# Kernel tuning notes

Hardware: AMD Instinct MI355X
Metric: run time of the kernel (lower is better)

The kernel has to match this reference:

```python
import jax, jax.numpy as jnp
import numpy as np

N = 50000   # nodes
E = 600000  # edges (avg degree 12)
F = 16      # raw node features
P = 32      # n_channels_preproc
C = 128     # n_channels
L = 6       # n_gnn_layers
LBL = 2     # n_labels


def _dense_init(k, fan_in, shape):
    return (jax.random.normal(k, shape, jnp.float32) / np.float32(np.sqrt(fan_in)))


def setup_inputs() -> dict:
    key = jax.random.key(0)
    ks = jax.random.split(key, 12)
    return {
        "x": jax.random.normal(ks[0], (N, F), jnp.float32),
        "edge_src": jax.random.randint(ks[1], (E,), 0, N, dtype=jnp.int32),
        "edge_dst": jax.random.randint(ks[2], (E,), 0, N, dtype=jnp.int32),
        "edge_weight": jax.random.uniform(ks[3], (E,), jnp.float32),  # normalized-adjacency values
        "preproc_W": _dense_init(ks[4], F, (F, P)), "preproc_b": jnp.zeros((P,), jnp.float32),
        "fc_in1_W": _dense_init(ks[5], P, (P, C)), "fc_in1_b": jnp.zeros((C,), jnp.float32),
        "fc_in2_W": _dense_init(ks[6], P, (P, C)), "fc_in2_b": jnp.zeros((C,), jnp.float32),
        "gcn_W": _dense_init(ks[7], C, (L, C, C)), "gcn_b": jnp.zeros((L, C), jnp.float32),
        "fcg_W": _dense_init(ks[8], 2 * C, (L, 2 * C, C)), "fcg_b": jnp.zeros((L, C), jnp.float32),
        "last1_W": _dense_init(ks[9], 2 * C, (2 * C, C)), "last1_b": jnp.zeros((C,), jnp.float32),
        "last2_W": _dense_init(ks[10], C, (C, LBL)), "last2_b": jnp.zeros((LBL,), jnp.float32),
    }


def reference(x, edge_src, edge_dst, edge_weight,
              preproc_W, preproc_b, fc_in1_W, fc_in1_b, fc_in2_W, fc_in2_b,
              gcn_W, gcn_b, fcg_W, fcg_b, last1_W, last1_b, last2_W, last2_b):
    relu = jax.nn.relu
    h = relu(x @ preproc_W + preproc_b)                      # preproc Dense
    node_id = relu(h @ fc_in1_W + fc_in1_b)                  # node identity branch
    h = relu(h @ fc_in2_W + fc_in2_b)

    def layer(h, params):
        W, b, Wf, bf = params
        # GCNConv: act(A_hat @ (h @ W) + b), A_hat as COO edge list
        hw = h @ W                                           # [N, C]
        msg = hw[edge_src] * edge_weight[:, None]            # [E, C]
        agg = jax.ops.segment_sum(msg, edge_dst, num_segments=N)
        g = relu(agg + b)
        merged = jnp.concatenate([node_id, g], axis=-1)      # [N, 2C]
        return relu(merged @ Wf + bf), None                  # dropout = identity (eval)

    h, _ = jax.lax.scan(layer, h, (gcn_W, gcn_b, fcg_W, fcg_b))

    merged = jnp.concatenate([node_id, h], axis=-1)
    h = relu(merged @ last1_W + last1_b)
    return jax.nn.sigmoid(h @ last2_W + last2_b)             # [N, n_labels]
```

## Files before the change

### kernel.cpp

```cpp
#include <hip/hip_runtime.h>
#include <cstddef>
#include <cstdint>

#define NN 50000
#define NE 600000
#define NB 391

typedef __attribute__((ext_vector_type(8))) short bf16x8;
typedef __attribute__((ext_vector_type(4))) float f32x4;

#define SWZ(x) (((x) ^ ((x) >> 2)) & 3)

#define GLDS16(src, dst)                                                     \
    __builtin_amdgcn_global_load_lds(                                        \
        (const __attribute__((address_space(1))) void*)(src),                \
        (__attribute__((address_space(3))) void*)(dst), 16, 0, 0)

__device__ __forceinline__ float bf2f(ushort u) {
    return __uint_as_float(((uint32_t)u) << 16);
}
__device__ __forceinline__ ushort f2bf(float f) {
    uint32_t b = __float_as_uint(f);
    return (ushort)((b + 0x7FFF + ((b >> 16) & 1)) >> 16);
}

__global__ __launch_bounds__(256)
void convbh_kernel(const float* __restrict__ f1W, const float* __restrict__ f2W,
                   const float* __restrict__ gW, const float* __restrict__ fgW,
                   const float* __restrict__ l1W, ushort* __restrict__ wt,
                   const int* __restrict__ dst, int* __restrict__ bcnt)
{
    if (blockIdx.x < 1312) {
        int i = blockIdx.x * 256 + threadIdx.x;
        if (i >= 335872) return;
        float v;
        if (i < 4096) {
            int c = i >> 5, k = i & 31;
            v = f1W[k * 128 + c];
        } else if (i < 8192) {
            int j = i - 4096; int c = j >> 5, k = j & 31;
            v = f2W[k * 128 + c];
        } else if (i < 8192 + 98304) {
            int j = i - 8192; int l = j >> 14, r = j & 16383;
            int c = r >> 7, k = r & 127;
            v = gW[l * 16384 + k * 128 + c];
        } else if (i < 8192 + 98304 + 196608) {
            int j = i - (8192 + 98304); int l = j >> 15, r = j & 32767;
            int c = r >> 8, k = r & 255;
            v = fgW[l * 32768 + k * 128 + c];
        } else {
            int j = i - (8192 + 98304 + 196608);
            int c = j >> 8, k = j & 255;
            v = l1W[k * 128 + c];
        }
        wt[i] = f2bf(v);
    } else {
        __shared__ int h[NB];
        int tx = threadIdx.x;
        for (int i = tx; i < NB; i += 256) h[i] = 0;
        __syncthreads();
        int e0 = (blockIdx.x - 1312) * 1024;
#pragma unroll
        for (int k = 0; k < 4; ++k) {
            int e = e0 + k * 256 + tx;
            if (e < NE) atomicAdd(&h[dst[e] >> 7], 1);
        }
        __syncthreads();
        for (int i = tx; i < NB; i += 256)
            if (h[i]) atomicAdd(&bcnt[i], h[i]);
    }
}

__global__ __launch_bounds__(512)
void bscan_kernel(const int* __restrict__ bcnt, int* __restrict__ bbase,
                  int* __restrict__ bcur)
{
    __shared__ int buf[512];
    int t = threadIdx.x;
    int v = (t < NB) ? bcnt[t] : 0;
    buf[t] = v;
    __syncthreads();
    for (int s = 1; s < 512; s <<= 1) {
        int u = (t >= s) ? buf[t - s] : 0;
        __syncthreads();
        buf[t] += u;
        __syncthreads();
    }
    if (t < NB) {
        int ex = buf[t] - v;
        bbase[t] = ex;
        bcur[t]  = ex;
    }
    if (t == 0) bbase[NB] = NE;
}

__global__ __launch_bounds__(256)
void pass1_kernel(const int* __restrict__ src, const int* __restrict__ dst,
                  const float* __restrict__ w, int* __restrict__ bcur,
                  unsigned int* __restrict__ stage_pk,
                  unsigned char* __restrict__ stage_dl)
{
    __shared__ int cnt[NB];
    __shared__ int gbase[NB];
    int tx = threadIdx.x;
    for (int i = tx; i < NB; i += 256) cnt[i] = 0;
    __syncthreads();
    int e0 = blockIdx.x * 1024;
    int myd[4], myrank[4];
    unsigned int mypk[4];
#pragma unroll
    for (int k = 0; k < 4; ++k) {
        int e = e0 + k * 256 + tx;
        if (e < NE) {
            int d = dst[e];
            myd[k]    = d;
            mypk[k]   = (unsigned int)src[e] | ((unsigned int)f2bf(w[e]) << 17);
            myrank[k] = atomicAdd(&cnt[d >> 7], 1);
        } else {
            myd[k] = -1;
        }
    }
    __syncthreads();
    for (int i = tx; i < NB; i += 256)
        gbase[i] = cnt[i] ? atomicAdd(&bcur[i], cnt[i]) : 0;
    __syncthreads();
#pragma unroll
    for (int k = 0; k < 4; ++k) {
        if (myd[k] >= 0) {
            int p = gbase[myd[k] >> 7] + myrank[k];
            stage_pk[p] = mypk[k];
            stage_dl[p] = (unsigned char)(myd[k] & 127);
        }
    }
}

__global__ __launch_bounds__(256)
void p2pre_kernel(const unsigned int* __restrict__ stage_pk,
                  const unsigned char* __restrict__ stage_dl,
                  const int* __restrict__ bbase,
                  unsigned int* __restrict__ esw, int* __restrict__ off,
                  const float* __restrict__ x, const float* __restrict__ preW,
                  const float* __restrict__ preb, ushort* __restrict__ h0b)
{
    if (blockIdx.x < NB) {
        __shared__ int h[128];
        __shared__ int lofs[128];
        int b    = blockIdx.x;
        int tx   = threadIdx.x;
        int base = bbase[b];
        int cnt  = bbase[b + 1] - base;
        if (tx < 128) h[tx] = 0;
        __syncthreads();
        for (int i = tx; i < cnt; i += 256)
            atomicAdd(&h[stage_dl[base + i]], 1);
        __syncthreads();
        if (tx == 0) {
            int run = 0;
            for (int i = 0; i < 128; ++i) { lofs[i] = run; run += h[i]; }
        }
        __syncthreads();
        int node0 = b * 128;
        if (tx < 128) {
            int n = node0 + tx;
            if (n < NN) off[n] = base + lofs[tx];
            h[tx] = 0;
        }
        if (b == NB - 1 && tx == 0) off[NN] = NE;
        __syncthreads();
        for (int i = tx; i < cnt; i += 256) {
            int d = stage_dl[base + i];
            int r = atomicAdd(&h[d], 1);
            esw[base + lofs[d] + r] = stage_pk[base + i];
        }
    } else {
        __shared__ float Wl[512];
        __shared__ float bl[32];
        int tx = threadIdx.x;
        Wl[tx]       = preW[tx];
        Wl[tx + 256] = preW[tx + 256];
        if (tx < 32) bl[tx] = preb[tx];
        __syncthreads();
        int n = (blockIdx.x - NB) * 256 + tx;
        if (n >= NN) return;
        float xr[16];
        const float4* xp = (const float4*)(x + (size_t)n * 16);
#pragma unroll
        for (int q = 0; q < 4; ++q) {
            float4 v = xp[q];
            xr[q*4+0]=v.x; xr[q*4+1]=v.y; xr[q*4+2]=v.z; xr[q*4+3]=v.w;
        }
        float acc[32];
#pragma unroll
        for (int c = 0; c < 32; ++c) acc[c] = bl[c];
#pragma unroll
        for (int k = 0; k < 16; ++k)
#pragma unroll
            for (int c = 0; c < 32; ++c)
                acc[c] = fmaf(xr[k], Wl[k*32+c], acc[c]);
        ushort4* op = (ushort4*)(h0b + (size_t)n * 32);
#pragma unroll
        for (int q = 0; q < 8; ++q) {
            ushort4 v;
            v.x = f2bf(fmaxf(acc[q*4+0], 0.f));
            v.y = f2bf(fmaxf(acc[q*4+1], 0.f));
            v.z = f2bf(fmaxf(acc[q*4+2], 0.f));
            v.w = f2bf(fmaxf(acc[q*4+3], 0.f));
            op[q] = v;
        }
    }
}

__global__ __launch_bounds__(128)
void fc1f0_kernel(const ushort* __restrict__ h0b,
                  const ushort* __restrict__ wf1, const float* __restrict__ f1b,
                  ushort* __restrict__ nidb,
                  const ushort* __restrict__ wf2, const float* __restrict__ f2b,
                  const ushort* __restrict__ wg, ushort* __restrict__ hwb)
{
    __shared__ ushort Atile[64 * 32];
    __shared__ ushort Btile[128 * 32];
    __shared__ ushort Xt[64 * 128];
    const int tx   = threadIdx.x;
    const int wave = tx >> 6;
    const int lane = tx & 63;
    const int rs  = lane >> 2;
    const int chn = (lane & 3) ^ SWZ(rs);
    const int m    = lane & 15;
    const int quad = lane >> 4;
    const int slot = quad ^ SWZ(m);

    if (blockIdx.x < 782) {
        const int bm = blockIdx.x * 64;
        f32x4 acc0[8], acc1[8];
#pragma unroll
        for (int t = 0; t < 8; ++t) {
            acc0[t] = (f32x4){0.f, 0.f, 0.f, 0.f};
            acc1[t] = (f32x4){0.f, 0.f, 0.f, 0.f};
        }
#pragma unroll
        for (int i = 0; i < 2; ++i) {
            int seg = wave + 2 * i;
            int row = seg * 16 + rs;
            int ar  = bm + row; if (ar >= NN) ar = NN - 1;
            GLDS16(h0b + (size_t)ar * 32 + chn * 8, Atile + seg * 512);
        }
#pragma unroll
        for (int i = 0; i < 4; ++i) {
            int seg = wave + 2 * i;
            int col = seg * 16 + rs;
            GLDS16(wf1 + (size_t)col * 32 + chn * 8, Btile + seg * 512);
        }
        __syncthreads();
        bf16x8 af0 = *(const bf16x8*)(Atile + (wave * 32 + m) * 32 + slot * 8);
        bf16x8 af1 = *(const bf16x8*)(Atile + (wave * 32 + 16 + m) * 32 + slot * 8);
#pragma unroll
        for (int t = 0; t < 8; ++t) {
            bf16x8 bfr = *(const bf16x8*)(Btile + (t * 16 + m) * 32 + slot * 8);
            acc0[t] = __builtin_amdgcn_mfma_f32_16x16x32_bf16(af0, bfr, acc0[t], 0, 0, 0);
            acc1[t] = __builtin_amdgcn_mfma_f32_16x16x32_bf16(af1, bfr, acc1[t], 0, 0, 0);
        }
        __syncthreads();
#pragma unroll
        for (int half = 0; half < 2; ++half) {
            const int orow0 = bm + wave * 32 + half * 16 + quad * 4;
#pragma unroll
            for (int t = 0; t < 8; ++t) {
                int col = t * 16 + m;
                float bb = f1b[col];
                f32x4 a = half ? acc1[t] : acc0[t];
#pragma unroll
                for (int r = 0; r < 4; ++r) {
                    int row = orow0 + r;
                    if (row < NN)
                        nidb[(size_t)row * 128 + col] = f2bf(fmaxf(a[r] + bb, 0.f));
                }
            }
        }
    } else {
        const int bm = (blockIdx.x - 782) * 64;
        f32x4 acc0[8], acc1[8];
#pragma unroll
        for (int t = 0; t < 8; ++t) {
            acc0[t] = (f32x4){0.f, 0.f, 0.f, 0.f};
            acc1[t] = (f32x4){0.f, 0.f, 0.f, 0.f};
        }
#pragma unroll
        for (int i = 0; i < 2; ++i) {
            int seg = wave + 2 * i;
            int row = seg * 16 + rs;
            int ar  = bm + row; if (ar >= NN) ar = NN - 1;
            GLDS16(h0b + (size_t)ar * 32 + chn * 8, Atile + seg * 512);
        }
#pragma unroll
        for (int i = 0; i < 4; ++i) {
            int seg = wave + 2 * i;
            int col = seg * 16 + rs;
            GLDS16(wf2 + (size_t)col * 32 + chn * 8, Btile + seg * 512);
        }
        __syncthreads();
        {
            bf16x8 af0 = *(const bf16x8*)(Atile + (wave * 32 + m) * 32 + slot * 8);
            bf16x8 af1 = *(const bf16x8*)(Atile + (wave * 32 + 16 + m) * 32 + slot * 8);
#pragma unroll
            for (int t = 0; t < 8; ++t) {
                bf16x8 bfr = *(const bf16x8*)(Btile + (t * 16 + m) * 32 + slot * 8);
                acc0[t] = __builtin_amdgcn_mfma_f32_16x16x32_bf16(af0, bfr, acc0[t], 0, 0, 0);
                acc1[t] = __builtin_amdgcn_mfma_f32_16x16x32_bf16(af1, bfr, acc1[t], 0, 0, 0);
            }
        }
        __syncthreads();
#pragma unroll
        for (int half = 0; half < 2; ++half) {
            int rbase = wave * 32 + half * 16 + quad * 4;
#pragma unroll
            for (int t = 0; t < 8; ++t) {
                int col = t * 16 + m;
                float bb = f2b[col];
                int c32 = col >> 5, within = col & 7, ks = (col >> 3) & 3;
                f32x4 a = half ? acc1[t] : acc0[t];
#pragma unroll
                for (int r = 0; r < 4; ++r) {
                    int row = rbase + r;
                    int pos = ks ^ SWZ(row & 15);
                    Xt[row * 128 + c32 * 32 + pos * 8 + within] =
                        f2bf(fmaxf(a[r] + bb, 0.f));
                }
            }
        }
#pragma unroll
        for (int t = 0; t < 8; ++t) {
            acc0[t] = (f32x4){0.f, 0.f, 0.f, 0.f};
            acc1[t] = (f32x4){0.f, 0.f, 0.f, 0.f};
        }
        __syncthreads();
        for (int c32 = 0; c32 < 4; ++c32) {
            int kk = c32 * 32;
#pragma unroll
            for (int i = 0; i < 4; ++i) {
                int seg = wave + 2 * i;
                int col = seg * 16 + rs;
                GLDS16(wg + (size_t)col * 128 + kk + chn * 8, Btile + seg * 512);
            }
            __syncthreads();
            bf16x8 af0 = *(const bf16x8*)(Xt + (wave * 32 + m) * 128 + kk + slot * 8);
            bf16x8 af1 = *(const bf16x8*)(Xt + (wave * 32 + 16 + m) * 128 + kk + slot * 8);
#pragma unroll
            for (int t = 0; t < 8; ++t) {
                bf16x8 bfr = *(const bf16x8*)(Btile + (t * 16 + m) * 32 + slot * 8);
                acc0[t] = __builtin_amdgcn_mfma_f32_16x16x32_bf16(af0, bfr, acc0[t], 0, 0, 0);
                acc1[t] = __builtin_amdgcn_mfma_f32_16x16x32_bf16(af1, bfr, acc1[t], 0, 0, 0);
            }
            __syncthreads();
        }
#pragma unroll
        for (int half = 0; half < 2; ++half) {
            const int orow0 = bm + wave * 32 + half * 16 + quad * 4;
#pragma unroll
            for (int t = 0; t < 8; ++t) {
                int col = t * 16 + m;
                f32x4 a = half ? acc1[t] : acc0[t];
#pragma unroll
                for (int r = 0; r < 4; ++r) {
                    int row = orow0 + r;
                    if (row < NN)
                        hwb[(size_t)row * 128 + col] = f2bf(a[r]);
                }
            }
        }
    }
}

__global__ __launch_bounds__(512)
void gemm_gather(const ushort* __restrict__ hw,
                 const unsigned int* __restrict__ esw,
                 const int* __restrict__ off,
                 const float* __restrict__ gbias,
                 const ushort* __restrict__ nid,
                 const ushort* __restrict__ Wt,
                 const float* __restrict__ bias,
                 const ushort* __restrict__ Wg,
                 ushort* __restrict__ out_hw, int nrows)
{
    __shared__ ushort Atile[64 * 32];
    __shared__ ushort Btile[128 * 32];
    __shared__ ushort AggXt[64 * 128];
    const int tx   = threadIdx.x;
    const int wave = tx >> 6;
    const int lane = tx & 63;
    const int bm   = blockIdx.x * 64;
    const int g    = wave >> 1;
    const int h    = wave & 1;
    const int rs   = lane >> 2;
    const int chn  = (lane & 3) ^ SWZ(rs);
    const int m    = lane & 15;
    const int quad = lane >> 4;
    const int slot = quad ^ SWZ(m);

    if (wave < 4) {
        int ar = bm + wave * 16 + rs; if (ar >= nrows) ar = nrows - 1;
        GLDS16(nid + (size_t)ar * 128 + chn * 8, Atile + wave * 512);
    }
    {
        int col = wave * 16 + rs;
        GLDS16(Wt + (size_t)col * 256 + chn * 8, Btile + wave * 512);
    }

    {
        const int n0   = bm + wave * 8;
        const int nend = n0 + 8;
        int n    = n0;
        const int base = off[n0 < NN ? n0 : NN];
        const int end  = off[nend < NN ? nend : NN];
        int nb = (n < NN) ? off[n + 1] : 0x7fffffff;
        const ushort* hp = hw + lane * 2;
        const float g0 = gbias[lane * 2], g1 = gbias[lane * 2 + 1];
        float a0 = 0.f, a1 = 0.f;
        const int c32g = lane >> 4;
        const int ksg  = (lane >> 2) & 3;
        const int wth  = (2 * lane) & 7;
        for (int chunk = base; chunk < end; chunk += 64) {
            int idx = chunk + lane;
            int pk = (idx < end) ? (int)esw[idx] : 0;
            int cnt = end - chunk; if (cnt > 64) cnt = 64;
            int cnt16 = (cnt + 15) & ~15;
            for (int j = 0; j < cnt16; j += 16) {
                int pp[16];
                unsigned int rv[16];
#pragma unroll
                for (int k = 0; k < 16; ++k)
                    pp[k] = __builtin_amdgcn_readlane(pk, j + k);
#pragma unroll
                for (int k = 0; k < 16; ++k)
                    rv[k] = *(const unsigned int*)(hp + (size_t)(pp[k] & 0x1FFFF) * 128);
#pragma unroll
                for (int k = 0; k < 16; ++k) {
                    int e = chunk + j + k;
                    while (e == nb) {
                        int row = n - bm;
                        unsigned int o = (unsigned int)f2bf(fmaxf(a0 + g0, 0.f)) |
                                         ((unsigned int)f2bf(fmaxf(a1 + g1, 0.f)) << 16);
                        int pos = ksg ^ SWZ(row & 15);
                        *(unsigned int*)(AggXt + row * 128 +
                            ((c32g * 32 + pos * 8 + wth) ^ ((row & 1) << 5))) = o;
                        a0 = 0.f; a1 = 0.f;
                        ++n;
                        nb = (n < nend && n < NN) ? off[n + 1] : 0x7fffffff;
                    }
                    float w = bf2f((ushort)((unsigned int)pp[k] >> 17));
                    a0 = fmaf(bf2f((ushort)(rv[k] & 0xffff)), w, a0);
                    a1 = fmaf(bf2f((ushort)(rv[k] >> 16)),    w, a1);
                }
            }
        }
        while (n < nend) {
            int row = n - bm;
            unsigned int o = (unsigned int)f2bf(fmaxf(a0 + g0, 0.f)) |
                             ((unsigned int)f2bf(fmaxf(a1 + g1, 0.f)) << 16);
            int pos = ksg ^ SWZ(row & 15);
            *(unsigned int*)(AggXt + row * 128 +
                ((c32g * 32 + pos * 8 + wth) ^ ((row & 1) << 5))) = o;
            a0 = 0.f; a1 = 0.f;
            ++n;
        }
    }

    f32x4 acc[4];
#pragma unroll
    for (int t = 0; t < 4; ++t) acc[t] = (f32x4){0.f, 0.f, 0.f, 0.f};

    for (int c8 = 0; c8 < 8; ++c8) {
        int kk = c8 * 32;
        if (c8 > 0) {
            if (c8 < 4 && wave < 4) {
                int ar = bm + wave * 16 + rs; if (ar >= nrows) ar = nrows - 1;
                GLDS16(nid + (size_t)ar * 128 + kk + chn * 8, Atile + wave * 512);
            }
            int col = wave * 16 + rs;
            GLDS16(Wt + (size_t)col * 256 + kk + chn * 8, Btile + wave * 512);
        }
        __syncthreads();
        bf16x8 af;
        if (c8 < 4) {
            af = *(const bf16x8*)(Atile + (g * 16 + m) * 32 + slot * 8);
        } else {
            int row = g * 16 + m;
            af = *(const bf16x8*)(AggXt + row * 128 +
                 (((c8 - 4) * 32 + slot * 8) ^ ((row & 1) << 5)));
        }
#pragma unroll
        for (int t = 0; t < 4; ++t) {
            bf16x8 bfr = *(const bf16x8*)(Btile + (h * 64 + t * 16 + m) * 32 + slot * 8);
            acc[t] = __builtin_amdgcn_mfma_f32_16x16x32_bf16(af, bfr, acc[t], 0, 0, 0);
        }
        __syncthreads();
    }

    {
        int col = wave * 16 + rs;
        GLDS16(Wg + (size_t)col * 128 + chn * 8, Btile + wave * 512);
    }

    {
        int rbase = g * 16 + quad * 4;
#pragma unroll
        for (int t = 0; t < 4; ++t) {
            int col = h * 64 + t * 16 + m;
            float bb = bias[col];
            int c32 = col >> 5, within = col & 7, ks = (col >> 3) & 3;
#pragma unroll
            for (int r = 0; r < 4; ++r) {
                int row = rbase + r;
                int pos = ks ^ SWZ(row & 15);
                AggXt[row * 128 + ((c32 * 32 + pos * 8 + within) ^ ((row & 1) << 5))] =
                    f2bf(fmaxf(acc[t][r] + bb, 0.f));
            }
        }
    }
#pragma unroll
    for (int t = 0; t < 4; ++t) acc[t] = (f32x4){0.f, 0.f, 0.f, 0.f};

    for (int c4 = 0; c4 < 4; ++c4) {
        int kk = c4 * 32;
        if (c4 > 0) {
            int col = wave * 16 + rs;
            GLDS16(Wg + (size_t)col * 128 + kk + chn * 8, Btile + wave * 512);
        }
        __syncthreads();
        int row = g * 16 + m;
        bf16x8 af = *(const bf16x8*)(AggXt + row * 128 +
                    ((kk + slot * 8) ^ ((row & 1) << 5)));
#pragma unroll
        for (int t = 0; t < 4; ++t) {
            bf16x8 bfr = *(const bf16x8*)(Btile + (h * 64 + t * 16 + m) * 32 + slot * 8);
            acc[t] = __builtin_amdgcn_mfma_f32_16x16x32_bf16(af, bfr, acc[t], 0, 0, 0);
        }
        __syncthreads();
    }

    {
        const int orow0 = bm + g * 16 + quad * 4;
#pragma unroll
        for (int t = 0; t < 4; ++t) {
            int col = h * 64 + t * 16 + m;
#pragma unroll
            for (int r = 0; r < 4; ++r) {
                int row = orow0 + r;
                if (row < nrows)
                    out_hw[(size_t)row * 128 + col] = f2bf(acc[t][r]);
            }
        }
    }
}

__global__ __launch_bounds__(512)
void gemm_last(const ushort* __restrict__ hw,
               const unsigned int* __restrict__ esw,
               const int* __restrict__ off,
               const float* __restrict__ gbias,
               const ushort* __restrict__ nid,
               const ushort* __restrict__ Wt, const float* __restrict__ bias5,
               const ushort* __restrict__ Wl1, const float* __restrict__ l1b,
               const float* __restrict__ l2W, const float* __restrict__ l2b,
               float* __restrict__ out, int nrows)
{
    __shared__ ushort Atile[64 * 32];
    __shared__ ushort Btile[128 * 32];
    __shared__ ushort AggXt[64 * 128];
    __shared__ float  w2s[256];
    __shared__ float  pbuf[64][2];
    const int tx   = threadIdx.x;
    const int wave = tx >> 6;
    const int lane = tx & 63;
    const int bm   = blockIdx.x * 64;
    const int g    = wave >> 1;
    const int h    = wave & 1;
    const int rs   = lane >> 2;
    const int chn  = (lane & 3) ^ SWZ(rs);
    const int m    = lane & 15;
    const int quad = lane >> 4;
    const int slot = quad ^ SWZ(m);

    if (tx < 256) w2s[tx] = l2W[tx];

    if (wave < 4) {
        int ar = bm + wave * 16 + rs; if (ar >= nrows) ar = nrows - 1;
        GLDS16(nid + (size_t)ar * 128 + chn * 8, Atile + wave * 512);
    }
    {
        int col = wave * 16 + rs;
        GLDS16(Wt + (size_t)col * 256 + chn * 8, Btile + wave * 512);
    }

    {
        const int n0   = bm + wave * 8;
        const int nend = n0 + 8;
        int n    = n0;
        const int base = off[n0 < NN ? n0 : NN];
        const int end  = off[nend < NN ? nend : NN];
        int nb = (n < NN) ? off[n + 1] : 0x7fffffff;
        const ushort* hp = hw + lane * 2;
        const float g0 = gbias[lane * 2], g1 = gbias[lane * 2 + 1];
        float a0 = 0.f, a1 = 0.f;
        const int c32g = lane >> 4;
        const int ksg  = (lane >> 2) & 3;
        const int wth  = (2 * lane) & 7;
        for (int chunk = base; chunk < end; chunk += 64) {
            int idx = chunk + lane;
            int pk = (idx < end) ? (int)esw[idx] : 0;
            int cnt = end - chunk; if (cnt > 64) cnt = 64;
            int cnt16 = (cnt + 15) & ~15;
            for (int j = 0; j < cnt16; j += 16) {
                int pp[16];
                unsigned int rv[16];
#pragma unroll
                for (int k = 0; k < 16; ++k)
                    pp[k] = __builtin_amdgcn_readlane(pk, j + k);
#pragma unroll
                for (int k = 0; k < 16; ++k)
                    rv[k] = *(const unsigned int*)(hp + (size_t)(pp[k] & 0x1FFFF) * 128);
#pragma unroll
                for (int k = 0; k < 16; ++k) {
                    int e = chunk + j + k;
                    while (e == nb) {
                        int row = n - bm;
                        unsigned int o = (unsigned int)f2bf(fmaxf(a0 + g0, 0.f)) |
                                         ((unsigned int)f2bf(fmaxf(a1 + g1, 0.f)) << 16);
                        int pos = ksg ^ SWZ(row & 15);
                        *(unsigned int*)(AggXt + row * 128 +
                            ((c32g * 32 + pos * 8 + wth) ^ ((row & 1) << 5))) = o;
                        a0 = 0.f; a1 = 0.f;
                        ++n;
                        nb = (n < nend && n < NN) ? off[n + 1] : 0x7fffffff;
                    }
                    float w = bf2f((ushort)((unsigned int)pp[k] >> 17));
                    a0 = fmaf(bf2f((ushort)(rv[k] & 0xffff)), w, a0);
                    a1 = fmaf(bf2f((ushort)(rv[k] >> 16)),    w, a1);
                }
            }
        }
        while (n < nend) {
            int row = n - bm;
            unsigned int o = (unsigned int)f2bf(fmaxf(a0 + g0, 0.f)) |
                             ((unsigned int)f2bf(fmaxf(a1 + g1, 0.f)) << 16);
            int pos = ksg ^ SWZ(row & 15);
            *(unsigned int*)(AggXt + row * 128 +
                ((c32g * 32 + pos * 8 + wth) ^ ((row & 1) << 5))) = o;
            a0 = 0.f; a1 = 0.f;
            ++n;
        }
    }

    f32x4 acc[4];
#pragma unroll
    for (int t = 0; t < 4; ++t) acc[t] = (f32x4){0.f, 0.f, 0.f, 0.f};

    for (int c8 = 0; c8 < 8; ++c8) {
        int kk = c8 * 32;
        if (c8 > 0) {
            if (c8 < 4 && wave < 4) {
                int ar = bm + wave * 16 + rs; if (ar >= nrows) ar = nrows - 1;
                GLDS16(nid + (size_t)ar * 128 + kk + chn * 8, Atile + wave * 512);
            }
            int col = wave * 16 + rs;
            GLDS16(Wt + (size_t)col * 256 + kk + chn * 8, Btile + wave * 512);
        }
        __syncthreads();
        bf16x8 af;
        if (c8 < 4) {
            af = *(const bf16x8*)(Atile + (g * 16 + m) * 32 + slot * 8);
        } else {
            int row = g * 16 + m;
            af = *(const bf16x8*)(AggXt + row * 128 +
                 (((c8 - 4) * 32 + slot * 8) ^ ((row & 1) << 5)));
        }
#pragma unroll
        for (int t = 0; t < 4; ++t) {
            bf16x8 bfr = *(const bf16x8*)(Btile + (h * 64 + t * 16 + m) * 32 + slot * 8);
            acc[t] = __builtin_amdgcn_mfma_f32_16x16x32_bf16(af, bfr, acc[t], 0, 0, 0);
        }
        __syncthreads();
    }

    if (wave < 4) {
        int ar = bm + wave * 16 + rs; if (ar >= nrows) ar = nrows - 1;
        GLDS16(nid + (size_t)ar * 128 + chn * 8, Atile + wave * 512);
    }
    {
        int col = wave * 16 + rs;
        GLDS16(Wl1 + (size_t)col * 256 + chn * 8, Btile + wave * 512);
    }

    {
        int rbase = g * 16 + quad * 4;
#pragma unroll
        for (int t = 0; t < 4; ++t) {
            int col = h * 64 + t * 16 + m;
            float bb = bias5[col];
            int c32 = col >> 5, within = col & 7, ks = (col >> 3) & 3;
#pragma unroll
            for (int r = 0; r < 4; ++r) {
                int row = rbase + r;
                int pos = ks ^ SWZ(row & 15);
                AggXt[row * 128 + ((c32 * 32 + pos * 8 + within) ^ ((row & 1) << 5))] =
                    f2bf(fmaxf(acc[t][r] + bb, 0.f));
            }
        }
    }
#pragma unroll
    for (int t = 0; t < 4; ++t) acc[t] = (f32x4){0.f, 0.f, 0.f, 0.f};

    for (int c8 = 0; c8 < 8; ++c8) {
        int kk = c8 * 32;
        if (c8 > 0) {
            if (c8 < 4 && wave < 4) {
                int ar = bm + wave * 16 + rs; if (ar >= nrows) ar = nrows - 1;
                GLDS16(nid + (size_t)ar * 128 + kk + chn * 8, Atile + wave * 512);
            }
            int col = wave * 16 + rs;
            GLDS16(Wl1 + (size_t)col * 256 + kk + chn * 8, Btile + wave * 512);
        }
        __syncthreads();
        bf16x8 af;
        if (c8 < 4) {
            af = *(const bf16x8*)(Atile + (g * 16 + m) * 32 + slot * 8);
        } else {
            int row = g * 16 + m;
            af = *(const bf16x8*)(AggXt + row * 128 +
                 (((c8 - 4) * 32 + slot * 8) ^ ((row & 1) << 5)));
        }
#pragma unroll
        for (int t = 0; t < 4; ++t) {
            bf16x8 bfr = *(const bf16x8*)(Btile + (h * 64 + t * 16 + m) * 32 + slot * 8);
            acc[t] = __builtin_amdgcn_mfma_f32_16x16x32_bf16(af, bfr, acc[t], 0, 0, 0);
        }
        __syncthreads();
    }

    float bb[4];
#pragma unroll
    for (int t = 0; t < 4; ++t) bb[t] = l1b[h * 64 + t * 16 + m];
    float pr0[4], pr1[4];
#pragma unroll
    for (int r = 0; r < 4; ++r) {
        float p0 = 0.f, p1 = 0.f;
#pragma unroll
        for (int t = 0; t < 4; ++t) {
            int col = h * 64 + t * 16 + m;
            float v = fmaxf(acc[t][r] + bb[t], 0.f);
            p0 = fmaf(v, w2s[col * 2 + 0], p0);
            p1 = fmaf(v, w2s[col * 2 + 1], p1);
        }
#pragma unroll
        for (int mask = 1; mask < 16; mask <<= 1) {
            p0 += __shfl_xor(p0, mask);
            p1 += __shfl_xor(p1, mask);
        }
        pr0[r] = p0; pr1[r] = p1;
    }
    if (h == 1 && m == 0) {
#pragma unroll
        for (int r = 0; r < 4; ++r) {
            int lrow = g * 16 + quad * 4 + r;
            pbuf[lrow][0] = pr0[r];
            pbuf[lrow][1] = pr1[r];
        }
    }
    __syncthreads();
    if (h == 0 && m == 0) {
        float b20 = l2b[0], b21 = l2b[1];
#pragma unroll
        for (int r = 0; r < 4; ++r) {
            int lrow = g * 16 + quad * 4 + r;
            int row = bm + lrow;
            if (row < nrows) {
                float p0 = pr0[r] + pbuf[lrow][0] + b20;
                float p1 = pr1[r] + pbuf[lrow][1] + b21;
                out[(size_t)row * 2 + 0] = 1.f / (1.f + __expf(-p0));
                out[(size_t)row * 2 + 1] = 1.f / (1.f + __expf(-p1));
            }
        }
    }
}

extern "C" void kernel_launch(void* const* d_in, const int* in_sizes, int n_in,
                              void* d_out, int out_size, void* d_ws, size_t ws_size,
                              hipStream_t stream)
{
    const float* x    = (const float*)d_in[0];
    const int*   esrc = (const int*)  d_in[1];
    const int*   edst = (const int*)  d_in[2];
    const float* ew   = (const float*)d_in[3];
    const float* preW = (const float*)d_in[4];
    const float* preb = (const float*)d_in[5];
    const float* f1W  = (const float*)d_in[6];
    const float* f1b  = (const float*)d_in[7];
    const float* f2W  = (const float*)d_in[8];
    const float* f2b  = (const float*)d_in[9];
    const float* gW   = (const float*)d_in[10];
    const float* gb   = (const float*)d_in[11];
    const float* fgW  = (const float*)d_in[12];
    const float* fgb  = (const float*)d_in[13];
    const float* l1W  = (const float*)d_in[14];
    const float* l1b  = (const float*)d_in[15];
    const float* l2W  = (const float*)d_in[16];
    const float* l2b  = (const float*)d_in[17];
    float* out = (float*)d_out;

    ushort* wt   = (ushort*)d_ws;
    ushort* wf1  = wt;
    ushort* wf2  = wf1 + 4096;
    ushort* wg   = wf2 + 4096;
    ushort* wfg  = wg  + 98304;
    ushort* wl1  = wfg + 196608;
    ushort* h0b  = wl1 + 32768;
    ushort* nidb = h0b  + (size_t)NN * 32;
    ushort* hwb  = nidb + (size_t)NN * 128;
    ushort* hwb2 = hwb  + (size_t)NN * 128;
    ushort* endu = hwb2 + (size_t)NN * 128;
    unsigned int* esw      = (unsigned int*)(((uintptr_t)endu + 15) & ~(uintptr_t)15);
    unsigned int* stage_pk = esw + NE;
    int*          bcnt     = (int*)(stage_pk + NE);
    int*          bbase    = bcnt + NB + 1;
    int*          bcur     = bbase + NB + 1;
    int*          off      = bcur + NB + 1;
    unsigned char* stage_dl = (unsigned char*)(off + NN + 2);

    const int gblocks = (NN + 63) / 64;
    const int eblocks = (NE + 1023) / 1024;

    hipMemsetAsync(bcnt, 0, (size_t)NB * sizeof(int), stream);
    convbh_kernel<<<1312 + eblocks, 256, 0, stream>>>(f1W, f2W, gW, fgW, l1W, wt,
                                                      edst, bcnt);
    bscan_kernel<<<1, 512, 0, stream>>>(bcnt, bbase, bcur);
    pass1_kernel<<<eblocks, 256, 0, stream>>>(esrc, edst, ew, bcur, stage_pk, stage_dl);
    p2pre_kernel<<<NB + (NN + 255) / 256, 256, 0, stream>>>(stage_pk, stage_dl, bbase,
                                                            esw, off, x, preW, preb, h0b);

    fc1f0_kernel<<<2 * gblocks, 128, 0, stream>>>(h0b, wf1, f1b, nidb,
                                                  wf2, f2b, wg, hwb);
    ushort* cur = hwb;
    ushort* nxt = hwb2;
    for (int l = 0; l < 5; ++l) {
        gemm_gather<<<gblocks, 512, 0, stream>>>(cur, esw, off,
                                                 gb + (size_t)l * 128, nidb,
                                                 wfg + (size_t)l * 32768,
                                                 fgb + (size_t)l * 128,
                                                 wg + (size_t)(l + 1) * 16384,
                                                 nxt, NN);
        ushort* tmp = cur; cur = nxt; nxt = tmp;
    }
    gemm_last<<<gblocks, 512, 0, stream>>>(cur, esw, off,
                                           gb + (size_t)5 * 128, nidb,
                                           wfg + (size_t)5 * 32768,
                                           fgb + (size_t)5 * 128,
                                           wl1, l1b, l2W, l2b, out, NN);
}
```

Measured before the change: 374.7 us.

## Double K-step to 64 in fused gather-GEMM kernels, scalarize edge reads

The fused gather+GEMM kernels now stage 64-wide K slices of A and B into larger LDS tiles, which halves the number of barrier-separated MFMA steps. The edge gather loop now reads packed edge words through readfirstlane scalar loads in groups of 16, replacing the per-lane chunk load followed by readlane broadcast. Offsets are also made wave-uniform. Launch bounds add an occupancy hint, and gemm_last drops its small LDS arrays by reading l2W directly and reusing Atile for the partial sums. The cost is more LDS per block and more global-load instructions per stage.

After: 461.1 us. 23.1% more time.

```diff
diff --git a/kernel.cpp b/kernel.cpp
--- a/kernel.cpp
+++ b/kernel.cpp
@@ -370,7 +370,7 @@
     }
 }
 
-__global__ __launch_bounds__(512)
+__global__ __launch_bounds__(512, 8)
 void gemm_gather(const ushort* __restrict__ hw,
                  const unsigned int* __restrict__ esw,
                  const int* __restrict__ off,
@@ -381,11 +381,11 @@
                  const ushort* __restrict__ Wg,
                  ushort* __restrict__ out_hw, int nrows)
 {
-    __shared__ ushort Atile[64 * 32];
-    __shared__ ushort Btile[128 * 32];
+    __shared__ ushort Atile[64 * 64];
+    __shared__ ushort Btile[128 * 64];
     __shared__ ushort AggXt[64 * 128];
     const int tx   = threadIdx.x;
-    const int wave = tx >> 6;
+    const int wave = __builtin_amdgcn_readfirstlane(tx >> 6);
     const int lane = tx & 63;
     const int bm   = blockIdx.x * 64;
     const int g    = wave >> 1;
@@ -396,63 +396,100 @@
     const int quad = lane >> 4;
     const int slot = quad ^ SWZ(m);
 
-    if (wave < 4) {
-        int ar = bm + wave * 16 + rs; if (ar >= nrows) ar = nrows - 1;
-        GLDS16(nid + (size_t)ar * 128 + chn * 8, Atile + wave * 512);
-    }
+    const int ac  = wave >> 2, asg = wave & 3;
+    int aar = bm + asg * 16 + rs; if (aar >= nrows) aar = nrows - 1;
+
+    auto stageA = [&](int koff) {
+        GLDS16(nid + (size_t)aar * 128 + koff + ac * 32 + chn * 8,
+               Atile + ac * 2048 + asg * 512);
+    };
+    auto stageB = [&](const ushort* W, int ldk, int koff) {
+#pragma unroll
+        for (int i = 0; i < 2; ++i) {
+            int u = wave + 8 * i, c = u >> 3, sg = u & 7;
+            int col = sg * 16 + rs;
+            GLDS16(W + (size_t)col * ldk + koff + c * 32 + chn * 8,
+                   Btile + c * 4096 + sg * 512);
+        }
+    };
+
+    f32x4 acc[4];
+#pragma unroll
+    for (int t = 0; t < 4; ++t) acc[t] = (f32x4){0.f, 0.f, 0.f, 0.f};
+
+    auto mfmaA = [&]() {
+#pragma unroll
+        for (int c = 0; c < 2; ++c) {
+            bf16x8 af = *(const bf16x8*)(Atile + c * 2048 + (g * 16 + m) * 32 + slot * 8);
+#pragma unroll
+            for (int t = 0; t < 4; ++t) {
+                bf16x8 bfr = *(const bf16x8*)(Btile + c * 4096 + (h * 64 + t * 16 + m) * 32 + slot * 8);
+                acc[t] = __builtin_amdgcn_mfma_f32_16x16x32_bf16(af, bfr, acc[t], 0, 0, 0);
+            }
+        }
+    };
+    auto mfmaX = [&](int x) {
+        const int row = g * 16 + m, rx = (row & 1) << 5;
+#pragma unroll
+        for (int c = 0; c < 2; ++c) {
+            bf16x8 af = *(const bf16x8*)(AggXt + row * 128 + (((x * 2 + c) * 32 + slot * 8) ^ rx));
+#pragma unroll
+            for (int t = 0; t < 4; ++t) {
+                bf16x8 bfr = *(const bf16x8*)(Btile + c * 4096 + (h * 64 + t * 16 + m) * 32 + slot * 8);
+                acc[t] = __builtin_amdgcn_mfma_f32_16x16x32_bf16(af, bfr, acc[t], 0, 0, 0);
+            }
+        }
+    };
+
+    stageA(0);
+    stageB(Wt, 256, 0);
+
     {
-        int col = wave * 16 + rs;
-        GLDS16(Wt + (size_t)col * 256 + chn * 8, Btile + wave * 512);
-    }
-
-    {
-        const int n0   = bm + wave * 8;
-        const int nend = n0 + 8;
-        int n    = n0;
-        const int base = off[n0 < NN ? n0 : NN];
-        const int end  = off[nend < NN ? nend : NN];
-        int nb = (n < NN) ? off[n + 1] : 0x7fffffff;
-        const ushort* hp = hw + lane * 2;
+        const int n0     = bm + wave * 8;
+        const int nend0  = n0 + 8;
+        const int nclamp = (nend0 < NN) ? nend0 : NN;
+        int n = n0;
+        const int base = __builtin_amdgcn_readfirstlane(off[(n0 < NN) ? n0 : NN]);
+        const int end  = __builtin_amdgcn_readfirstlane(off[nclamp]);
+        int nb = (n < nclamp) ? __builtin_amdgcn_readfirstlane(off[n + 1]) : 0x7fffffff;
         const float g0 = gbias[lane * 2], g1 = gbias[lane * 2 + 1];
         float a0 = 0.f, a1 = 0.f;
         const int c32g = lane >> 4;
         const int ksg  = (lane >> 2) & 3;
         const int wth  = (2 * lane) & 7;
-        for (int chunk = base; chunk < end; chunk += 64) {
-            int idx = chunk + lane;
-            int pk = (idx < end) ? (int)esw[idx] : 0;
-            int cnt = end - chunk; if (cnt > 64) cnt = 64;
-            int cnt16 = (cnt + 15) & ~15;
-            for (int j = 0; j < cnt16; j += 16) {
-                int pp[16];
-                unsigned int rv[16];
-#pragma unroll
-                for (int k = 0; k < 16; ++k)
-                    pp[k] = __builtin_amdgcn_readlane(pk, j + k);
-#pragma unroll
-                for (int k = 0; k < 16; ++k)
-                    rv[k] = *(const unsigned int*)(hp + (size_t)(pp[k] & 0x1FFFF) * 128);
-#pragma unroll
-                for (int k = 0; k < 16; ++k) {
-                    int e = chunk + j + k;
-                    while (e == nb) {
-                        int row = n - bm;
-                        unsigned int o = (unsigned int)f2bf(fmaxf(a0 + g0, 0.f)) |
-                                         ((unsigned int)f2bf(fmaxf(a1 + g1, 0.f)) << 16);
-                        int pos = ksg ^ SWZ(row & 15);
-                        *(unsigned int*)(AggXt + row * 128 +
-                            ((c32g * 32 + pos * 8 + wth) ^ ((row & 1) << 5))) = o;
-                        a0 = 0.f; a1 = 0.f;
-                        ++n;
-                        nb = (n < nend && n < NN) ? off[n + 1] : 0x7fffffff;
-                    }
-                    float w = bf2f((ushort)((unsigned int)pp[k] >> 17));
-                    a0 = fmaf(bf2f((ushort)(rv[k] & 0xffff)), w, a0);
-                    a1 = fmaf(bf2f((ushort)(rv[k] >> 16)),    w, a1);
+        for (int e0 = base; e0 < end; e0 += 16) {
+            unsigned int pks[16];
+#pragma unroll
+            for (int k = 0; k < 16; ++k)
+                pks[k] = __builtin_amdgcn_readfirstlane(
+                    (e0 + k < end) ? esw[e0 + k] : 0u);
+            unsigned int rv[16];
+#pragma unroll
+            for (int k = 0; k < 16; ++k)
+                rv[k] = *(const unsigned int*)(
+                    hw + (((size_t)(pks[k] & 0x1FFFFu)) << 7) + lane * 2);
+#pragma unroll
+            for (int k = 0; k < 16; ++k) {
+                int e = e0 + k;
+                if (e >= end) break;
+                while (e == nb) {
+                    int row = n - bm;
+                    unsigned int o = (unsigned int)f2bf(fmaxf(a0 + g0, 0.f)) |
+                                     ((unsigned int)f2bf(fmaxf(a1 + g1, 0.f)) << 16);
+                    int pos = ksg ^ SWZ(row & 15);
+                    *(unsigned int*)(AggXt + row * 128 +
+                        ((c32g * 32 + pos * 8 + wth) ^ ((row & 1) << 5))) = o;
+                    a0 = 0.f; a1 = 0.f;
+                    ++n;
+                    nb = (n < nclamp) ? __builtin_amdgcn_readfirstlane(off[n + 1])
+                                      : 0x7fffffff;
                 }
-            }
-        }
-        while (n < nend) {
+                float w = bf2f((ushort)(pks[k] >> 17));
+                a0 = fmaf(bf2f((ushort)(rv[k] & 0xffffu)), w, a0);
+                a1 = fmaf(bf2f((ushort)(rv[k] >> 16)), w, a1);
+            }
+        }
+        while (n < nend0) {
             int row = n - bm;
             unsigned int o = (unsigned int)f2bf(fmaxf(a0 + g0, 0.f)) |
                              ((unsigned int)f2bf(fmaxf(a1 + g1, 0.f)) << 16);
@@ -464,41 +501,23 @@
         }
     }
 
-    f32x4 acc[4];
-#pragma unroll
-    for (int t = 0; t < 4; ++t) acc[t] = (f32x4){0.f, 0.f, 0.f, 0.f};
-
-    for (int c8 = 0; c8 < 8; ++c8) {
-        int kk = c8 * 32;
-        if (c8 > 0) {
-            if (c8 < 4 && wave < 4) {
-                int ar = bm + wave * 16 + rs; if (ar >= nrows) ar = nrows - 1;
-                GLDS16(nid + (size_t)ar * 128 + kk + chn * 8, Atile + wave * 512);
-            }
-            int col = wave * 16 + rs;
-            GLDS16(Wt + (size_t)col * 256 + kk + chn * 8, Btile + wave * 512);
-        }
-        __syncthreads();
-        bf16x8 af;
-        if (c8 < 4) {
-            af = *(const bf16x8*)(Atile + (g * 16 + m) * 32 + slot * 8);
-        } else {
-            int row = g * 16 + m;
-            af = *(const bf16x8*)(AggXt + row * 128 +
-                 (((c8 - 4) * 32 + slot * 8) ^ ((row & 1) << 5)));
-        }
-#pragma unroll
-        for (int t = 0; t < 4; ++t) {
-            bf16x8 bfr = *(const bf16x8*)(Btile + (h * 64 + t * 16 + m) * 32 + slot * 8);
-            acc[t] = __builtin_amdgcn_mfma_f32_16x16x32_bf16(af, bfr, acc[t], 0, 0, 0);
-        }
-        __syncthreads();
-    }
-
-    {
-        int col = wave * 16 + rs;
-        GLDS16(Wg + (size_t)col * 128 + chn * 8, Btile + wave * 512);
-    }
+    __syncthreads();
+    mfmaA();
+    __syncthreads();
+    stageA(64); stageB(Wt, 256, 64);
+    __syncthreads();
+    mfmaA();
+    __syncthreads();
+    stageB(Wt, 256, 128);
+    __syncthreads();
+    mfmaX(0);
+    __syncthreads();
+    stageB(Wt, 256, 192);
+    __syncthreads();
+    mfmaX(1);
+    __syncthreads();
+
+    stageB(Wg, 128, 0);
 
     {
         int rbase = g * 16 + quad * 4;
@@ -518,24 +537,13 @@
     }
 #pragma unroll
     for (int t = 0; t < 4; ++t) acc[t] = (f32x4){0.f, 0.f, 0.f, 0.f};
-
-    for (int c4 = 0; c4 < 4; ++c4) {
-        int kk = c4 * 32;
-        if (c4 > 0) {
-            int col = wave * 16 + rs;
-            GLDS16(Wg + (size_t)col * 128 + kk + chn * 8, Btile + wave * 512);
-        }
-        __syncthreads();
-        int row = g * 16 + m;
-        bf16x8 af = *(const bf16x8*)(AggXt + row * 128 +
-                    ((kk + slot * 8) ^ ((row & 1) << 5)));
-#pragma unroll
-        for (int t = 0; t < 4; ++t) {
-            bf16x8 bfr = *(const bf16x8*)(Btile + (h * 64 + t * 16 + m) * 32 + slot * 8);
-            acc[t] = __builtin_amdgcn_mfma_f32_16x16x32_bf16(af, bfr, acc[t], 0, 0, 0);
-        }
-        __syncthreads();
-    }
+    __syncthreads();
+
+    mfmaX(0);
+    __syncthreads();
+    stageB(Wg, 128, 64);
+    __syncthreads();
+    mfmaX(1);
 
     {
         const int orow0 = bm + g * 16 + quad * 4;
@@ -552,7 +560,7 @@
     }
 }
 
-__global__ __launch_bounds__(512)
+__global__ __launch_bounds__(512, 8)
 void gemm_last(const ushort* __restrict__ hw,
                const unsigned int* __restrict__ esw,
                const int* __restrict__ off,
@@ -563,13 +571,11 @@
                const float* __restrict__ l2W, const float* __restrict__ l2b,
                float* __restrict__ out, int nrows)
 {
-    __shared__ ushort Atile[64 * 32];
-    __shared__ ushort Btile[128 * 32];
+    __shared__ ushort Atile[64 * 64];
+    __shared__ ushort Btile[128 * 64];
     __shared__ ushort AggXt[64 * 128];
-    __shared__ float  w2s[256];
-    __shared__ float  pbuf[64][2];
     const int tx   = threadIdx.x;
-    const int wave = tx >> 6;
+    const int wave = __builtin_amdgcn_readfirstlane(tx >> 6);
     const int lane = tx & 63;
     const int bm   = blockIdx.x * 64;
     const int g    = wave >> 1;
@@ -580,65 +586,100 @@
     const int quad = lane >> 4;
     const int slot = quad ^ SWZ(m);
 
-    if (tx < 256) w2s[tx] = l2W[tx];
-
-    if (wave < 4) {
-        int ar = bm + wave * 16 + rs; if (ar >= nrows) ar = nrows - 1;
-        GLDS16(nid + (size_t)ar * 128 + chn * 8, Atile + wave * 512);
-    }
+    const int ac  = wave >> 2, asg = wave & 3;
+    int aar = bm + asg * 16 + rs; if (aar >= nrows) aar = nrows - 1;
+
+    auto stageA = [&](int koff) {
+        GLDS16(nid + (size_t)aar * 128 + koff + ac * 32 + chn * 8,
+               Atile + ac * 2048 + asg * 512);
+    };
+    auto stageB = [&](const ushort* W, int ldk, int koff) {
+#pragma unroll
+        for (int i = 0; i < 2; ++i) {
+            int u = wave + 8 * i, c = u >> 3, sg = u & 7;
+            int col = sg * 16 + rs;
+            GLDS16(W + (size_t)col * ldk + koff + c * 32 + chn * 8,
+                   Btile + c * 4096 + sg * 512);
+        }
+    };
+
+    f32x4 acc[4];
+#pragma unroll
+    for (int t = 0; t < 4; ++t) acc[t] = (f32x4){0.f, 0.f, 0.f, 0.f};
+
+    auto mfmaA = [&]() {
+#pragma unroll
+        for (int c = 0; c < 2; ++c) {
+            bf16x8 af = *(const bf16x8*)(Atile + c * 2048 + (g * 16 + m) * 32 + slot * 8);
+#pragma unroll
+            for (int t = 0; t < 4; ++t) {
+                bf16x8 bfr = *(const bf16x8*)(Btile + c * 4096 + (h * 64 + t * 16 + m) * 32 + slot * 8);
+                acc[t] = __builtin_amdgcn_mfma_f32_16x16x32_bf16(af, bfr, acc[t], 0, 0, 0);
+            }
+        }
+    };
+    auto mfmaX = [&](int x) {
+        const int row = g * 16 + m, rx = (row & 1) << 5;
+#pragma unroll
+        for (int c = 0; c < 2; ++c) {
+            bf16x8 af = *(const bf16x8*)(AggXt + row * 128 + (((x * 2 + c) * 32 + slot * 8) ^ rx));
+#pragma unroll
+            for (int t = 0; t < 4; ++t) {
+                bf16x8 bfr = *(const bf16x8*)(Btile + c * 4096 + (h * 64 + t * 16 + m) * 32 + slot * 8);
+                acc[t] = __builtin_amdgcn_mfma_f32_16x16x32_bf16(af, bfr, acc[t], 0, 0, 0);
+            }
+        }
+    };
+
+    stageA(0);
+    stageB(Wt, 256, 0);
+
     {
-        int col = wave * 16 + rs;
-        GLDS16(Wt + (size_t)col * 256 + chn * 8, Btile + wave * 512);
-    }
-
-    {
-        const int n0   = bm + wave * 8;
-        const int nend = n0 + 8;
-        int n    = n0;
-        const int base = off[n0 < NN ? n0 : NN];
-        const int end  = off[nend < NN ? nend : NN];
-        int nb = (n < NN) ? off[n + 1] : 0x7fffffff;
-        const ushort* hp = hw + lane * 2;
+        const int n0     = bm + wave * 8;
+        const int nend0  = n0 + 8;
+        const int nclamp = (nend0 < NN) ? nend0 : NN;
+        int n = n0;
+        const int base = __builtin_amdgcn_readfirstlane(off[(n0 < NN) ? n0 : NN]);
+        const int end  = __builtin_amdgcn_readfirstlane(off[nclamp]);
+        int nb = (n < nclamp) ? __builtin_amdgcn_readfirstlane(off[n + 1]) : 0x7fffffff;
         const float g0 = gbias[lane * 2], g1 = gbias[lane * 2 + 1];
         float a0 = 0.f, a1 = 0.f;
         const int c32g = lane >> 4;
         const int ksg  = (lane >> 2) & 3;
         const int wth  = (2 * lane) & 7;
-        for (int chunk = base; chunk < end; chunk += 64) {
-            int idx = chunk + lane;
-            int pk = (idx < end) ? (int)esw[idx] : 0;
-            int cnt = end - chunk; if (cnt > 64) cnt = 64;
-            int cnt16 = (cnt + 15) & ~15;
-            for (int j = 0; j < cnt16; j += 16) {
-                int pp[16];
-                unsigned int rv[16];
-#pragma unroll
-                for (int k = 0; k < 16; ++k)
-                    pp[k] = __builtin_amdgcn_readlane(pk, j + k);
-#pragma unroll
-                for (int k = 0; k < 16; ++k)
-                    rv[k] = *(const unsigned int*)(hp + (size_t)(pp[k] & 0x1FFFF) * 128);
-#pragma unroll
-                for (int k = 0; k < 16; ++k) {
-                    int e = chunk + j + k;
-                    while (e == nb) {
-                        int row = n - bm;
-                        unsigned int o = (unsigned int)f2bf(fmaxf(a0 + g0, 0.f)) |
-                                         ((unsigned int)f2bf(fmaxf(a1 + g1, 0.f)) << 16);
-                        int pos = ksg ^ SWZ(row & 15);
-                        *(unsigned int*)(AggXt + row * 128 +
-                            ((c32g * 32 + pos * 8 + wth) ^ ((row & 1) << 5))) = o;
-                        a0 = 0.f; a1 = 0.f;
-                        ++n;
-                        nb = (n < nend && n < NN) ? off[n + 1] : 0x7fffffff;
-                    }
-                    float w = bf2f((ushort)((unsigned int)pp[k] >> 17));
-                    a0 = fmaf(bf2f((ushort)(rv[k] & 0xffff)), w, a0);
-                    a1 = fmaf(bf2f((ushort)(rv[k] >> 16)),    w, a1);
+        for (int e0 = base; e0 < end; e0 += 16) {
+            unsigned int pks[16];
+#pragma unroll
+            for (int k = 0; k < 16; ++k)
+                pks[k] = __builtin_amdgcn_readfirstlane(
+                    (e0 + k < end) ? esw[e0 + k] : 0u);
+            unsigned int rv[16];
+#pragma unroll
+            for (int k = 0; k < 16; ++k)
+                rv[k] = *(const unsigned int*)(
+                    hw + (((size_t)(pks[k] & 0x1FFFFu)) << 7) + lane * 2);
+#pragma unroll
+            for (int k = 0; k < 16; ++k) {
+                int e = e0 + k;
+                if (e >= end) break;
+                while (e == nb) {
+                    int row = n - bm;
+                    unsigned int o = (unsigned int)f2bf(fmaxf(a0 + g0, 0.f)) |
+                                     ((unsigned int)f2bf(fmaxf(a1 + g1, 0.f)) << 16);
+                    int pos = ksg ^ SWZ(row & 15);
+                    *(unsigned int*)(AggXt + row * 128 +
+                        ((c32g * 32 + pos * 8 + wth) ^ ((row & 1) << 5))) = o;
+                    a0 = 0.f; a1 = 0.f;
+                    ++n;
+                    nb = (n < nclamp) ? __builtin_amdgcn_readfirstlane(off[n + 1])
+                                      : 0x7fffffff;
                 }
-            }
-        }
-        while (n < nend) {
+                float w = bf2f((ushort)(pks[k] >> 17));
+                a0 = fmaf(bf2f((ushort)(rv[k] & 0xffffu)), w, a0);
+                a1 = fmaf(bf2f((ushort)(rv[k] >> 16)), w, a1);
+            }
+        }
+        while (n < nend0) {
             int row = n - bm;
             unsigned int o = (unsigned int)f2bf(fmaxf(a0 + g0, 0.f)) |
                              ((unsigned int)f2bf(fmaxf(a1 + g1, 0.f)) << 16);
@@ -650,45 +691,24 @@
         }
     }
 
-    f32x4 acc[4];
-#pragma unroll
-    for (int t = 0; t < 4; ++t) acc[t] = (f32x4){0.f, 0.f, 0.f, 0.f};
-
-    for (int c8 = 0; c8 < 8; ++c8) {
-        int kk = c8 * 32;
-        if (c8 > 0) {
-            if (c8 < 4 && wave < 4) {
-                int ar = bm + wave * 16 + rs; if (ar >= nrows) ar = nrows - 1;
-                GLDS16(nid + (size_t)ar * 128 + kk + chn * 8, Atile + wave * 512);
-            }
-            int col = wave * 16 + rs;
-            GLDS16(Wt + (size_t)col * 256 + kk + chn * 8, Btile + wave * 512);
-        }
-        __syncthreads();
-        bf16x8 af;
-        if (c8 < 4) {
-            af = *(const bf16x8*)(Atile + (g * 16 + m) * 32 + slot * 8);
-        } else {
-            int row = g * 16 + m;
-            af = *(const bf16x8*)(AggXt + row * 128 +
-                 (((c8 - 4) * 32 + slot * 8) ^ ((row & 1) << 5)));
-        }
-#pragma unroll
-        for (int t = 0; t < 4; ++t) {
-            bf16x8 bfr = *(const bf16x8*)(Btile + (h * 64 + t * 16 + m) * 32 + slot * 8);
-            acc[t] = __builtin_amdgcn_mfma_f32_16x16x32_bf16(af, bfr, acc[t], 0, 0, 0);
-        }
-        __syncthreads();
-    }
-
-    if (wave < 4) {
-        int ar = bm + wave * 16 + rs; if (ar >= nrows) ar = nrows - 1;
-        GLDS16(nid + (size_t)ar * 128 + chn * 8, Atile + wave * 512);
-    }
-    {
-        int col = wave * 16 + rs;
-        GLDS16(Wl1 + (size_t)col * 256 + chn * 8, Btile + wave * 512);
-    }
+    __syncthreads();
+    mfmaA();
+    __syncthreads();
+    stageA(64); stageB(Wt, 256, 64);
+    __syncthreads();
+    mfmaA();
+    __syncthreads();
+    stageB(Wt, 256, 128);
+    __syncthreads();
+    mfmaX(0);
+    __syncthreads();
+    stageB(Wt, 256, 192);
+    __syncthreads();
+    mfmaX(1);
+    __syncthreads();
+
+    stageA(0);
+    stageB(Wl1, 256, 0);
 
     {
         int rbase = g * 16 + quad * 4;
@@ -708,33 +728,21 @@
     }
 #pragma unroll
     for (int t = 0; t < 4; ++t) acc[t] = (f32x4){0.f, 0.f, 0.f, 0.f};
-
-    for (int c8 = 0; c8 < 8; ++c8) {
-        int kk = c8 * 32;
-        if (c8 > 0) {
-            if (c8 < 4 && wave < 4) {
-                int ar = bm + wave * 16 + rs; if (ar >= nrows) ar = nrows - 1;
-                GLDS16(nid + (size_t)ar * 128 + kk + chn * 8, Atile + wave * 512);
-            }
-            int col = wave * 16 + rs;
-            GLDS16(Wl1 + (size_t)col * 256 + kk + chn * 8, Btile + wave * 512);
-        }
-        __syncthreads();
-        bf16x8 af;
-        if (c8 < 4) {
-            af = *(const bf16x8*)(Atile + (g * 16 + m) * 32 + slot * 8);
-        } else {
-            int row = g * 16 + m;
-            af = *(const bf16x8*)(AggXt + row * 128 +
-                 (((c8 - 4) * 32 + slot * 8) ^ ((row & 1) << 5)));
-        }
-#pragma unroll
-        for (int t = 0; t < 4; ++t) {
-            bf16x8 bfr = *(const bf16x8*)(Btile + (h * 64 + t * 16 + m) * 32 + slot * 8);
-            acc[t] = __builtin_amdgcn_mfma_f32_16x16x32_bf16(af, bfr, acc[t], 0, 0, 0);
-        }
-        __syncthreads();
-    }
+    __syncthreads();
+
+    mfmaA();
+    __syncthreads();
+    stageA(64); stageB(Wl1, 256, 64);
+    __syncthreads();
+    mfmaA();
+    __syncthreads();
+    stageB(Wl1, 256, 128);
+    __syncthreads();
+    mfmaX(0);
+    __syncthreads();
+    stageB(Wl1, 256, 192);
+    __syncthreads();
+    mfmaX(1);
 
     float bb[4];
 #pragma unroll
@@ -747,8 +755,8 @@
         for (int t = 0; t < 4; ++t) {
             int col = h * 64 + t * 16 + m;
             float v = fmaxf(acc[t][r] + bb[t], 0.f);
-            p0 = fmaf(v, w2s[col * 2 + 0], p0);
-            p1 = fmaf(v, w2s[col * 2 + 1], p1);
+            p0 = fmaf(v, l2W[col * 2 + 0], p0);
+            p1 = fmaf(v, l2W[col * 2 + 1], p1);
         }
 #pragma unroll
         for (int mask = 1; mask < 16; mask <<= 1) {
@@ -757,12 +765,13 @@
         }
         pr0[r] = p0; pr1[r] = p1;
     }
+    float* pbuf = (float*)Atile;
     if (h == 1 && m == 0) {
 #pragma unroll
         for (int r = 0; r < 4; ++r) {
             int lrow = g * 16 + quad * 4 + r;
-            pbuf[lrow][0] = pr0[r];
-            pbuf[lrow][1] = pr1[r];
+            pbuf[lrow * 2 + 0] = pr0[r];
+            pbuf[lrow * 2 + 1] = pr1[r];
         }
     }
     __syncthreads();
@@ -773,8 +782,8 @@
             int lrow = g * 16 + quad * 4 + r;
             int row = bm + lrow;
             if (row < nrows) {
-                float p0 = pr0[r] + pbuf[lrow][0] + b20;
-                float p1 = pr1[r] + pbuf[lrow][1] + b21;
+                float p0 = pr0[r] + pbuf[lrow * 2 + 0] + b20;
+                float p1 = pr1[r] + pbuf[lrow * 2 + 1] + b21;
                 out[(size_t)row * 2 + 0] = 1.f / (1.f + __expf(-p0));
                 out[(size_t)row * 2 + 1] = 1.f / (1.f + __expf(-p1));
             }
```
